# Kernel optimization log

Hardware: AMD Instinct MI355X
Metric: run time of the kernel (lower is better)

The kernel has to match this reference:

```python
import jax, jax.numpy as jnp
import numpy as np

B, L, D = 2, 2048, 4096
H, KV, HD = 32, 8, 128          # query heads, kv heads, head_dim
G = H // KV                      # GQA group size
THETA = 10000.0
SCALE = HD ** -0.5


def apply_rope(x, offset=0):
    """Non-traditional (half-split) RoPE. x: [B, heads, L, HD]."""
    hd = x.shape[-1]
    half = hd // 2
    inv_freq = 1.0 / (THETA ** (jnp.arange(0, hd, 2, dtype=jnp.float32) / hd))  # [half]
    pos = jnp.arange(offset, offset + x.shape[2], dtype=jnp.float32)            # [L]
    ang = pos[:, None] * inv_freq[None, :]                                      # [L, half]
    cos = jnp.cos(ang).astype(x.dtype)
    sin = jnp.sin(ang).astype(x.dtype)
    x1, x2 = x[..., :half], x[..., half:]
    return jnp.concatenate([x1 * cos - x2 * sin, x2 * cos + x1 * sin], axis=-1)


def setup_inputs() -> dict:
    key = jax.random.key(0)
    ks = jax.random.split(key, 8)
    s = 0.02
    return {
        "x": jax.random.normal(ks[0], (B, L, D), dtype=jnp.float32),
        "Wq": jax.random.normal(ks[1], (D, H * HD), dtype=jnp.float32) * s,
        "bq": jnp.zeros((H * HD,), dtype=jnp.float32),
        "Wk": jax.random.normal(ks[2], (D, KV * HD), dtype=jnp.float32) * s,
        "bk": jnp.zeros((KV * HD,), dtype=jnp.float32),
        "Wv": jax.random.normal(ks[3], (D, KV * HD), dtype=jnp.float32) * s,
        "bv": jnp.zeros((KV * HD,), dtype=jnp.float32),
        "Wo": jax.random.normal(ks[4], (H * HD, D), dtype=jnp.float32) * s,
    }


def reference(x, Wq, bq, Wk, bk, Wv, bv, Wo):
    b, l, _ = x.shape
    # projections
    q = (x @ Wq + bq).reshape(b, l, H, HD).transpose(0, 2, 1, 3)   # [B,H,L,HD]
    k = (x @ Wk + bk).reshape(b, l, KV, HD).transpose(0, 2, 1, 3)  # [B,KV,L,HD]
    v = (x @ Wv + bv).reshape(b, l, KV, HD).transpose(0, 2, 1, 3)  # [B,KV,L,HD]
    # RoPE (cache=None path, offset 0)
    q = apply_rope(q)
    k = apply_rope(k)
    # GQA SDPA without materializing repeated KV heads
    qg = q.reshape(b, KV, G, l, HD)                                 # [B,KV,G,L,HD]
    scores = jnp.einsum('bkgld,bkmd->bkglm', qg, k) * SCALE         # [B,KV,G,L,L]
    probs = jax.nn.softmax(scores, axis=-1)
    out = jnp.einsum('bkglm,bkmd->bkgld', probs, v)                 # [B,KV,G,L,HD]
    out = out.reshape(b, H, l, HD).transpose(0, 2, 1, 3).reshape(b, l, H * HD)
    return out @ Wo
```

## Files before the change

kernel.cpp:

```cpp
#include <hip/hip_runtime.h>
#include <stdint.h>
#include <stddef.h>


typedef _Float16 half_t;
typedef __attribute__((ext_vector_type(4))) _Float16 f16x4;
typedef __attribute__((ext_vector_type(8))) _Float16 f16x8;
typedef __attribute__((ext_vector_type(4))) float f32x4;

#define NB 2
#define NL 2048
#define ND 4096
#define NH 32
#define NKV 8
#define NHD 128
#define NG 4
#define NQKV 6144
#define QK_SCALE 0.08838834764831845f
#define RLOG2E 1.4426950408889634f
#define M0 6.0f
#define THR 8.0f

static __device__ __forceinline__ void gll16(const void* g, void* l) {
  __builtin_amdgcn_global_load_lds(
      (__attribute__((address_space(1))) void*)(void*)(g),
      (__attribute__((address_space(3))) void*)(l),
      16, 0, 0);
}

__global__ void convert_f32_f16_kernel(const float* __restrict__ in,
                                       half_t* __restrict__ out, int n4) {
  int i = blockIdx.x * 256 + threadIdx.x;
  if (i >= n4) return;
  const float4 v = reinterpret_cast<const float4*>(in)[i];
  f16x4 o;
  o[0] = (half_t)v.x; o[1] = (half_t)v.y; o[2] = (half_t)v.z; o[3] = (half_t)v.w;
  reinterpret_cast<f16x4*>(out)[i] = o;
}

__global__ void wtrans_kernel(const float* __restrict__ W,
                              half_t* __restrict__ Wt, int K, int N) {
  __shared__ float tile[32][33];
  const int n0 = blockIdx.x * 32;
  const int k0 = blockIdx.y * 32;
  const int tx = threadIdx.x, ty = threadIdx.y;
#pragma unroll
  for (int r = 0; r < 32; r += 8)
    tile[ty + r][tx] = W[(size_t)(k0 + ty + r) * N + n0 + tx];
  __syncthreads();
#pragma unroll
  for (int r = 0; r < 32; r += 8)
    Wt[(size_t)(n0 + ty + r) * K + k0 + tx] = (half_t)tile[tx][ty + r];
}

template <typename OutT>
__global__ __launch_bounds__(512, 2) void gemm256_kernel(
    const half_t* __restrict__ A, const half_t* __restrict__ Bt,
    const float* __restrict__ B0, const float* __restrict__ B1,
    const float* __restrict__ B2, OutT* __restrict__ C,
    int M, int N, int K) {
  constexpr int BK = 32;
  __shared__ __align__(16) half_t As[4][256 * BK];
  __shared__ __align__(16) half_t Bs[4][256 * BK];

  const int tid = threadIdx.x;
  const int wave = tid >> 6, lane = tid & 63;
  const int r16 = lane & 15, quad = lane >> 4;
  const int wm = wave >> 2, wn = wave & 3;

  const int nbx = N >> 8;
  const int lid = (int)(blockIdx.y * gridDim.x + blockIdx.x);
  const int nwg = (int)(gridDim.x * gridDim.y);
  const int cpx = nwg >> 3;
  const int swz = (lid & 7) * cpx + (lid >> 3);
  const int brow = (swz / nbx) * 256;
  const int bcol = (swz % nbx) * 256;

  const int NT = K >> 5;

  auto stage = [&](int t) {
    const int buf = t & 3;
    const int k0 = t << 5;
#pragma unroll
    for (int j = 0; j < 2; ++j) {
      const int s = j * 512 + wave * 64 + lane;
      const int row = s >> 2;
      const int cg = (s & 3) ^ (row & 3);
      gll16(A  + (size_t)(brow + row) * K + k0 + cg * 8,
            &As[buf][(j * 512 + wave * 64) * 8]);
      gll16(Bt + (size_t)(bcol + row) * K + k0 + cg * 8,
            &Bs[buf][(j * 512 + wave * 64) * 8]);
    }
  };

  f32x4 acc[8][4] = {};

  stage(0); stage(1); stage(2);
  asm volatile("s_waitcnt vmcnt(8)" ::: "memory");
  __builtin_amdgcn_s_barrier();

  for (int t = 0; t < NT; ++t) {
    if (t > 0) {
      asm volatile("s_waitcnt lgkmcnt(0)" ::: "memory");
      __builtin_amdgcn_s_barrier();
    }
    if (t + 3 < NT) {
      stage(t + 3);
      asm volatile("s_waitcnt vmcnt(8)" ::: "memory");
    } else if (t + 2 < NT) {
      asm volatile("s_waitcnt vmcnt(4)" ::: "memory");
    } else if (t + 1 < NT) {
      asm volatile("s_waitcnt vmcnt(0)" ::: "memory");
    }

    const int buf = t & 3;
    const half_t* Ab = &As[buf][0];
    const half_t* Bb = &Bs[buf][0];
    const int csw = (quad ^ (r16 & 3)) << 3;

    f16x8 bf[4];
#pragma unroll
    for (int ni = 0; ni < 4; ++ni) {
      const int col = wn * 64 + ni * 16 + r16;
      bf[ni] = *reinterpret_cast<const f16x8*>(&Bb[col * BK + csw]);
    }
    __builtin_amdgcn_s_setprio(1);
#pragma unroll
    for (int mi = 0; mi < 8; ++mi) {
      const int row = wm * 128 + mi * 16 + r16;
      const f16x8 af = *reinterpret_cast<const f16x8*>(&Ab[row * BK + csw]);
#pragma unroll
      for (int ni = 0; ni < 4; ++ni)
        acc[mi][ni] = __builtin_amdgcn_mfma_f32_16x16x32_f16(
            af, bf[ni], acc[mi][ni], 0, 0, 0);
    }
    __builtin_amdgcn_s_setprio(0);
  }

#pragma unroll
  for (int ni = 0; ni < 4; ++ni) {
    const int col = bcol + wn * 64 + ni * 16 + r16;
    float bv = 0.0f;
    if (B0) bv = (col < ND) ? B0[col]
                            : (col < ND + NKV * NHD ? B1[col - ND]
                                                    : B2[col - ND - NKV * NHD]);
#pragma unroll
    for (int mi = 0; mi < 8; ++mi) {
      const int row0 = brow + wm * 128 + mi * 16 + quad * 4;
#pragma unroll
      for (int i = 0; i < 4; ++i)
        C[(size_t)(row0 + i) * N + col] = (OutT)(acc[mi][ni][i] + bv);
    }
  }
}

__global__ void ropepack_kernel(const half_t* __restrict__ rawh,
                                half_t* __restrict__ qb,
                                half_t* __restrict__ kb) {
  const size_t idx = (size_t)blockIdx.x * 256 + threadIdx.x;
  const int d = (int)(idx & 63);
  size_t t = idx >> 6;
  const int hp = (int)(t % (NH + NKV)); t /= (NH + NKV);
  const int l = (int)(t % NL);
  const int b = (int)(t / NL);
  const bool isQ = hp < NH;
  const int col0 = isQ ? hp * NHD : ND + (hp - NH) * NHD;
  const half_t* src = rawh + ((size_t)b * NL + l) * NQKV + col0;
  const float x1 = (float)src[d];
  const float x2 = (float)src[d + 64];
  const float inv_freq = exp2f(-(float)d * 0.20762050593045935f);
  const float ang = (float)l * inv_freq;
  float sn, cs;
  __sincosf(ang, &sn, &cs);
  const float scale = isQ ? QK_SCALE : 1.0f;
  half_t* dst = isQ ? qb + ((size_t)(b * NH + hp) * NL + l) * NHD
                    : kb + ((size_t)(b * NKV + (hp - NH)) * NL + l) * NHD;
  dst[d]      = (half_t)((x1 * cs - x2 * sn) * scale);
  dst[d + 64] = (half_t)((x2 * cs + x1 * sn) * scale);
}

__global__ void vtrans16_kernel(const half_t* __restrict__ rawh,
                                half_t* __restrict__ Vt) {
  __shared__ half_t tile[32][34];
  const int bkv = blockIdx.z;
  const int l0 = blockIdx.x * 32;
  const int d0 = blockIdx.y * 32;
  const int b = bkv / NKV, kvh = bkv % NKV;
  const int tx = threadIdx.x, ty = threadIdx.y;
#pragma unroll
  for (int r = 0; r < 32; r += 8)
    tile[ty + r][tx] = rawh[(size_t)(b * NL + l0 + ty + r) * NQKV
                            + ND + NKV * NHD + kvh * NHD + d0 + tx];
  __syncthreads();
  half_t* dst = Vt + (size_t)bkv * NHD * NL;
#pragma unroll
  for (int r = 0; r < 32; r += 8)
    dst[(size_t)(d0 + ty + r) * NL + l0 + tx] = tile[tx][ty + r];
}

#define KVB 64

__global__ __launch_bounds__(512, 2) void attn_kernel(
    const half_t* __restrict__ Q,
    const half_t* __restrict__ Kh,
    const half_t* __restrict__ Vt,
    half_t* __restrict__ O) {
  __shared__ half_t Ks[2][KVB * NHD];
  __shared__ half_t Vs[2][NHD * KVB];
  __shared__ half_t Ps[8][16 * 64];

  const int tid = threadIdx.x;
  const int wave = tid >> 6, lane = tid & 63;
  const int r16 = lane & 15, quad = lane >> 4;
  const int r7 = r16 & 7;

  const int bid = (int)blockIdx.x;
  const int swz = (bid & 7) * 64 + (bid >> 3);
  const int nqt = NL / 256;
  const int bh = swz / nqt, qt = swz % nqt;
  const int b = bh / NH, h = bh % NH;
  const int kvh = h / NG;

  const int qrow0 = qt * 256 + wave * 32;
  const half_t* Qb = Q  + ((size_t)(b * NH + h) * NL + qrow0) * NHD;
  const half_t* Kb = Kh + ((size_t)(b * NKV + kvh) * NL) * NHD;
  const half_t* Vb = Vt + ((size_t)(b * NKV + kvh) * NHD) * NL;
  half_t* Pw = &Ps[wave][0];

  auto stage = [&](int buf, int n0) {
#pragma unroll
    for (int j = 0; j < 2; ++j) {
      const int slot = j * 512 + wave * 64 + lane;
      {
        const int row = slot >> 4;
        const int c = (slot & 15) ^ (row & 7);
        gll16(Kb + (size_t)(n0 + row) * NHD + c * 8,
              &Ks[buf][(j * 512 + wave * 64) * 8]);
      }
      {
        const int row = slot >> 3;
        const int c = (slot & 7) ^ (row & 7);
        gll16(Vb + (size_t)row * NL + n0 + c * 8,
              &Vs[buf][(j * 512 + wave * 64) * 8]);
      }
    }
  };

  stage(0, 0);

  f16x8 qf[2][4];
#pragma unroll
  for (int rt = 0; rt < 2; ++rt)
#pragma unroll
    for (int c = 0; c < 4; ++c)
      qf[rt][c] = *reinterpret_cast<const f16x8*>(
          &Qb[(size_t)(rt * 16 + r16) * NHD + c * 32 + quad * 8]);

  f32x4 oacc[2][8];
  float m_run[2][4], lsum[2][4];
#pragma unroll
  for (int rt = 0; rt < 2; ++rt) {
#pragma unroll
    for (int i = 0; i < 4; ++i) { m_run[rt][i] = M0; lsum[rt][i] = 0.0f; }
#pragma unroll
    for (int dt = 0; dt < 8; ++dt) oacc[rt][dt] = (f32x4){0.f, 0.f, 0.f, 0.f};
  }

  const int swzread = r7 ^ ((r16 >> 3) * 5);

  asm volatile("s_waitcnt vmcnt(0)" ::: "memory");
  __syncthreads();

  int cur = 0;
  for (int t = 0; t < NL / KVB; ++t, cur ^= 1) {
    if (t + 1 < NL / KVB) stage(cur ^ 1, (t + 1) * KVB);

    const half_t* Kc = &Ks[cur][0];
    const half_t* Vc = &Vs[cur][0];

    f32x4 s[2][4] = {};
#pragma unroll
    for (int c = 0; c < 4; ++c) {
      const int ch = ((c * 4 + quad) ^ r7) * 8;
#pragma unroll
      for (int nt = 0; nt < 4; ++nt) {
        f16x8 kf = *reinterpret_cast<const f16x8*>(&Kc[(nt * 16 + r16) * NHD + ch]);
        s[0][nt] = __builtin_amdgcn_mfma_f32_16x16x32_f16(qf[0][c], kf, s[0][nt], 0, 0, 0);
        s[1][nt] = __builtin_amdgcn_mfma_f32_16x16x32_f16(qf[1][c], kf, s[1][nt], 0, 0, 0);
      }
    }

    float mx[2][4];
    bool need = false;
#pragma unroll
    for (int rt = 0; rt < 2; ++rt)
#pragma unroll
      for (int i = 0; i < 4; ++i) {
        mx[rt][i] = fmaxf(fmaxf(s[rt][0][i], s[rt][1][i]),
                          fmaxf(s[rt][2][i], s[rt][3][i]));
        need = need || (mx[rt][i] > m_run[rt][i] + THR);
      }
    if (__any(need ? 1 : 0)) {
#pragma unroll
      for (int rt = 0; rt < 2; ++rt)
#pragma unroll
        for (int i = 0; i < 4; ++i) {
          float m = mx[rt][i];
#pragma unroll
          for (int off = 1; off < 16; off <<= 1)
            m = fmaxf(m, __shfl_xor(m, off));
          const float mn = fmaxf(m_run[rt][i], m);
          const float corr = exp2f((m_run[rt][i] - mn) * RLOG2E);
          m_run[rt][i] = mn;
          lsum[rt][i] *= corr;
#pragma unroll
          for (int dt = 0; dt < 8; ++dt) oacc[rt][dt][i] *= corr;
        }
    }

    f16x8 pa[2][2];
#pragma unroll
    for (int rt = 0; rt < 2; ++rt) {
#pragma unroll
      for (int i = 0; i < 4; ++i) {
        const float mrl = m_run[rt][i] * RLOG2E;
        float p[4];
#pragma unroll
        for (int nt = 0; nt < 4; ++nt)
          p[nt] = exp2f(s[rt][nt][i] * RLOG2E - mrl);
        lsum[rt][i] += (p[0] + p[1]) + (p[2] + p[3]);
        const int row = quad * 4 + i;
        const int swzr = (row & 7) ^ ((row >> 3) * 5);
#pragma unroll
        for (int nt = 0; nt < 4; ++nt)
          Pw[row * 64 + (((nt * 2 + (r16 >> 3)) ^ swzr) * 8) + r7] = (half_t)p[nt];
      }
      pa[rt][0] = *reinterpret_cast<const f16x8*>(&Pw[r16 * 64 + ((quad ^ swzread) * 8)]);
      pa[rt][1] = *reinterpret_cast<const f16x8*>(&Pw[r16 * 64 + (((4 + quad) ^ swzread) * 8)]);
    }

    const int ch0 = (quad ^ r7) * 8;
    const int ch1 = ((4 + quad) ^ r7) * 8;
#pragma unroll
    for (int dt = 0; dt < 8; ++dt) {
      const int row = dt * 16 + r16;
      f16x8 v0 = *reinterpret_cast<const f16x8*>(&Vc[row * 64 + ch0]);
      f16x8 v1 = *reinterpret_cast<const f16x8*>(&Vc[row * 64 + ch1]);
      oacc[0][dt] = __builtin_amdgcn_mfma_f32_16x16x32_f16(pa[0][0], v0, oacc[0][dt], 0, 0, 0);
      oacc[0][dt] = __builtin_amdgcn_mfma_f32_16x16x32_f16(pa[0][1], v1, oacc[0][dt], 0, 0, 0);
      oacc[1][dt] = __builtin_amdgcn_mfma_f32_16x16x32_f16(pa[1][0], v0, oacc[1][dt], 0, 0, 0);
      oacc[1][dt] = __builtin_amdgcn_mfma_f32_16x16x32_f16(pa[1][1], v1, oacc[1][dt], 0, 0, 0);
    }

    asm volatile("s_waitcnt vmcnt(0)" ::: "memory");
    __syncthreads();
  }

  half_t* Ob = O + ((size_t)(b * NL) + qrow0) * (NH * NHD) + (size_t)h * NHD;
#pragma unroll
  for (int rt = 0; rt < 2; ++rt)
#pragma unroll
    for (int i = 0; i < 4; ++i) {
      float l = lsum[rt][i];
#pragma unroll
      for (int off = 1; off < 16; off <<= 1)
        l += __shfl_xor(l, off);
      const float inv = 1.0f / l;
      const int rl = rt * 16 + quad * 4 + i;
#pragma unroll
      for (int dt = 0; dt < 8; ++dt)
        Ob[(size_t)rl * (NH * NHD) + dt * 16 + r16] =
            (half_t)(oacc[rt][dt][i] * inv);
    }
}

extern "C" void kernel_launch(void* const* d_in, const int* in_sizes, int n_in,
                              void* d_out, int out_size, void* d_ws, size_t ws_size,
                              hipStream_t stream) {
  const float* x  = (const float*)d_in[0];
  const float* Wq = (const float*)d_in[1];
  const float* bq = (const float*)d_in[2];
  const float* Wk = (const float*)d_in[3];
  const float* bk = (const float*)d_in[4];
  const float* Wv = (const float*)d_in[5];
  const float* bv = (const float*)d_in[6];
  const float* Wo = (const float*)d_in[7];
  float* out = (float*)d_out;

  char* ws = (char*)d_ws;
  size_t off = 0;
  auto alloc = [&](size_t bytes) {
    size_t cur = off;
    off += (bytes + 255) & ~(size_t)255;
    return cur;
  };
  const size_t M = (size_t)NB * NL;
  half_t* xb   = (half_t*)(ws + alloc(M * ND * 2));
  half_t* wqkv = (half_t*)(ws + alloc((size_t)NQKV * ND * 2));
  half_t* rawh = (half_t*)(ws + alloc(M * NQKV * 2));
  half_t* qb   = (half_t*)(ws + alloc(M * (size_t)(NH * NHD) * 2));
  half_t* kb   = (half_t*)(ws + alloc(M * (size_t)(NKV * NHD) * 2));
  half_t* vt   = (half_t*)(ws + alloc(M * (size_t)(NKV * NHD) * 2));

  {
    int n4 = (int)(M * ND / 4);
    convert_f32_f16_kernel<<<dim3((n4 + 255) / 256), dim3(256), 0, stream>>>(x, xb, n4);
  }
  wtrans_kernel<<<dim3(ND / 32, ND / 32), dim3(32, 8), 0, stream>>>(
      Wq, wqkv, ND, ND);
  wtrans_kernel<<<dim3((NKV * NHD) / 32, ND / 32), dim3(32, 8), 0, stream>>>(
      Wk, wqkv + (size_t)ND * ND, ND, NKV * NHD);
  wtrans_kernel<<<dim3((NKV * NHD) / 32, ND / 32), dim3(32, 8), 0, stream>>>(
      Wv, wqkv + (size_t)(ND + NKV * NHD) * ND, ND, NKV * NHD);

  gemm256_kernel<half_t><<<dim3(NQKV / 256, M / 256), dim3(512), 0, stream>>>(
      xb, wqkv, bq, bk, bv, rawh, (int)M, NQKV, ND);

  ropepack_kernel<<<dim3((unsigned)(M * (NH + NKV) * 64 / 256)), dim3(256), 0, stream>>>(
      rawh, qb, kb);
  vtrans16_kernel<<<dim3(NL / 32, NHD / 32, NB * NKV), dim3(32, 8), 0, stream>>>(rawh, vt);

  wtrans_kernel<<<dim3(ND / 32, ND / 32), dim3(32, 8), 0, stream>>>(Wo, wqkv, NH * NHD, ND);

  attn_kernel<<<dim3(NB * NH * (NL / 256)), dim3(512), 0, stream>>>(qb, kb, vt, xb);

  gemm256_kernel<float><<<dim3(ND / 256, M / 256), dim3(512), 0, stream>>>(
      xb, wqkv, nullptr, nullptr, nullptr, out, (int)M, ND, ND);
}
```

Baseline: 775.4 us.

## Split GEMM k-step into two half phases interleaving A/B staging with MFMA

Restructures the GEMM main loop into two phases per k-tile. Each phase first issues LDS fragment reads, then prefetches half of the next global-to-LDS stage (A in the first phase, B in the second), then runs 16 MFMAs under raised priority. The phases are separated by workgroup barriers and sched_barriers. The aim is a ping-pong style schedule that overlaps global loads, LDS reads and matrix math more evenly, at the cost of more barriers per iteration and tighter ordering of the buffer-reuse hazards.

After: 685.4 us. 11.6% less time.

```diff
diff --git a/kernel.cpp b/kernel.cpp
--- a/kernel.cpp
+++ b/kernel.cpp
@@ -78,7 +78,7 @@
 
   const int NT = K >> 5;
 
-  auto stage = [&](int t) {
+  auto stageA = [&](int t) {
     const int buf = t & 3;
     const int k0 = t << 5;
 #pragma unroll
@@ -86,55 +86,85 @@
       const int s = j * 512 + wave * 64 + lane;
       const int row = s >> 2;
       const int cg = (s & 3) ^ (row & 3);
-      gll16(A  + (size_t)(brow + row) * K + k0 + cg * 8,
+      gll16(A + (size_t)(brow + row) * K + k0 + cg * 8,
             &As[buf][(j * 512 + wave * 64) * 8]);
+    }
+  };
+  auto stageB = [&](int t) {
+    const int buf = t & 3;
+    const int k0 = t << 5;
+#pragma unroll
+    for (int j = 0; j < 2; ++j) {
+      const int s = j * 512 + wave * 64 + lane;
+      const int row = s >> 2;
+      const int cg = (s & 3) ^ (row & 3);
       gll16(Bt + (size_t)(bcol + row) * K + k0 + cg * 8,
             &Bs[buf][(j * 512 + wave * 64) * 8]);
     }
   };
 
   f32x4 acc[8][4] = {};
-
-  stage(0); stage(1); stage(2);
+  const int csw = (quad ^ (r16 & 3)) << 3;
+
+  stageA(0); stageB(0); stageA(1); stageB(1); stageA(2); stageB(2);
   asm volatile("s_waitcnt vmcnt(8)" ::: "memory");
   __builtin_amdgcn_s_barrier();
 
   for (int t = 0; t < NT; ++t) {
-    if (t > 0) {
-      asm volatile("s_waitcnt lgkmcnt(0)" ::: "memory");
-      __builtin_amdgcn_s_barrier();
-    }
+    const int buf = t & 3;
+    const half_t* Ab = &As[buf][0];
+    const half_t* Bb = &Bs[buf][0];
+
+    f16x8 af[4], bf[4];
+#pragma unroll
+    for (int ni = 0; ni < 4; ++ni)
+      bf[ni] = *reinterpret_cast<const f16x8*>(
+          &Bb[(wn * 64 + ni * 16 + r16) * BK + csw]);
+#pragma unroll
+    for (int mi = 0; mi < 4; ++mi)
+      af[mi] = *reinterpret_cast<const f16x8*>(
+          &Ab[(wm * 128 + mi * 16 + r16) * BK + csw]);
+    if (t + 3 < NT) stageA(t + 3);
+    __builtin_amdgcn_sched_barrier(0);
+    __builtin_amdgcn_s_barrier();
+    asm volatile("s_waitcnt lgkmcnt(0)" ::: "memory");
+    __builtin_amdgcn_sched_barrier(0);
+    __builtin_amdgcn_s_setprio(1);
+#pragma unroll
+    for (int mi = 0; mi < 4; ++mi)
+#pragma unroll
+      for (int ni = 0; ni < 4; ++ni)
+        acc[mi][ni] = __builtin_amdgcn_mfma_f32_16x16x32_f16(
+            af[mi], bf[ni], acc[mi][ni], 0, 0, 0);
+    __builtin_amdgcn_s_setprio(0);
+    __builtin_amdgcn_s_barrier();
+
+    f16x8 ah[4];
+#pragma unroll
+    for (int mi = 0; mi < 4; ++mi)
+      ah[mi] = *reinterpret_cast<const f16x8*>(
+          &Ab[(wm * 128 + 64 + mi * 16 + r16) * BK + csw]);
+    if (t + 3 < NT) stageB(t + 3);
     if (t + 3 < NT) {
-      stage(t + 3);
       asm volatile("s_waitcnt vmcnt(8)" ::: "memory");
     } else if (t + 2 < NT) {
       asm volatile("s_waitcnt vmcnt(4)" ::: "memory");
     } else if (t + 1 < NT) {
       asm volatile("s_waitcnt vmcnt(0)" ::: "memory");
     }
-
-    const int buf = t & 3;
-    const half_t* Ab = &As[buf][0];
-    const half_t* Bb = &Bs[buf][0];
-    const int csw = (quad ^ (r16 & 3)) << 3;
-
-    f16x8 bf[4];
-#pragma unroll
-    for (int ni = 0; ni < 4; ++ni) {
-      const int col = wn * 64 + ni * 16 + r16;
-      bf[ni] = *reinterpret_cast<const f16x8*>(&Bb[col * BK + csw]);
-    }
+    __builtin_amdgcn_sched_barrier(0);
+    __builtin_amdgcn_s_barrier();
+    asm volatile("s_waitcnt lgkmcnt(0)" ::: "memory");
+    __builtin_amdgcn_sched_barrier(0);
     __builtin_amdgcn_s_setprio(1);
 #pragma unroll
-    for (int mi = 0; mi < 8; ++mi) {
-      const int row = wm * 128 + mi * 16 + r16;
-      const f16x8 af = *reinterpret_cast<const f16x8*>(&Ab[row * BK + csw]);
+    for (int mi = 0; mi < 4; ++mi)
 #pragma unroll
       for (int ni = 0; ni < 4; ++ni)
-        acc[mi][ni] = __builtin_amdgcn_mfma_f32_16x16x32_f16(
-            af, bf[ni], acc[mi][ni], 0, 0, 0);
-    }
+        acc[mi + 4][ni] = __builtin_amdgcn_mfma_f32_16x16x32_f16(
+            ah[mi], bf[ni], acc[mi + 4][ni], 0, 0, 0);
     __builtin_amdgcn_s_setprio(0);
+    __builtin_amdgcn_s_barrier();
   }
 
 #pragma unroll
```
